# Optimization experiments

Measured on AMD Instinct MI355X. Metric: run time of the kernel, lower is better.

Reference implementation:

```python
import jax, jax.numpy as jnp
import numpy as np

# NOTE on reconstructed deps (not shown in source):
#  - utils.mmnorm(x): max-magnitude norm, x / (max|x| over last dim + eps)
#  - model.LearnableFourierResampler(din, dout, nf): x -> Linear(din,nf) -> [sin,cos] -> Linear(2nf,dout)
#  - utils.pscan(q, fn, identity): Hillis-Steele log-depth scan: for n in 1,2,4,...:
#        q = fn(x=q, y=shift_right(q, n, fill=identity))   (Scanner.forward(x, y) cats (y, x))

B, T, C, NF = 8, 2048, 1024, 64
EPS = 1e-6

def mmnorm(x):
    return x / (jnp.max(jnp.abs(x), axis=-1, keepdims=True) + EPS)

def setup_inputs() -> dict:
    key = jax.random.key(0)
    ks = jax.random.split(key, 8)
    def w(k, shape, fan_in):
        return jax.random.normal(k, shape, jnp.float32) * (1.0 / np.sqrt(fan_in))
    return {
        "x": jax.random.normal(ks[0], (B, T, C), jnp.float32),
        "attn_W": w(ks[1], (C, 2 * C), C),
        "attn_b": jnp.zeros((2 * C,), jnp.float32),
        "freq_W": w(ks[2], (2 * C, NF), 2 * C),
        "freq_b": jnp.zeros((NF,), jnp.float32),
        "out_W": w(ks[3], (2 * NF, C), 2 * NF),
        "out_b": jnp.zeros((C,), jnp.float32),
        "proj_W": w(ks[4], (C, C), C),
        "proj_b": jnp.zeros((C,), jnp.float32),
        "identity": jax.random.uniform(ks[5], (C,), jnp.float32),
    }

def _scanner(y, x, freq_W, freq_b, out_W, out_b):
    # Scanner.forward(x, y): z = cat((y, x)); Fourier resample; mmnorm
    z = jnp.concatenate([y, x], axis=-1)                      # [B,T,2C]
    f = z @ freq_W + freq_b                                   # [B,T,NF]
    z = jnp.concatenate([jnp.sin(f), jnp.cos(f)], -1) @ out_W + out_b  # [B,T,C]
    return mmnorm(z)

def reference(x, attn_W, attn_b, freq_W, freq_b, out_W, out_b, proj_W, proj_b, identity):
    b, t, c = x.shape
    qv = x @ attn_W + attn_b
    q, v = qv[..., :c], qv[..., c:]
    # Hillis-Steele parallel scan with nonlinear learned combine
    n = 1
    while n < t:
        prev = jnp.concatenate(
            [jnp.broadcast_to(identity, (b, n, c)), q[:, : t - n]], axis=1)
        q = _scanner(prev, q, freq_W, freq_b, out_W, out_b)
        n *= 2
    Y = q * v
    return Y @ proj_W + proj_b
```

## Files before the change

kernel.cpp:

```cpp
#include <hip/hip_runtime.h>
#include <hip/hip_bf16.h>
#include <math.h>


#define R_ROWS 16384
#define T_DIM  2048
#define C_DIM  1024

typedef unsigned short u16;
typedef __attribute__((ext_vector_type(8))) short short8;
typedef __attribute__((ext_vector_type(4))) float f32x4;

__device__ __forceinline__ u16 f2bf(float f) {
  union { float f; unsigned u; } v; v.f = f;
  unsigned r = v.u + 0x7fffu + ((v.u >> 16) & 1u);
  return (u16)(r >> 16);
}
__device__ __forceinline__ float bf2f(u16 h) {
  union { unsigned u; float f; } v; v.u = ((unsigned)h) << 16;
  return v.f;
}
__device__ __forceinline__ void gld16(const void* g, void* l) {
  __builtin_amdgcn_global_load_lds(
      (const __attribute__((address_space(1))) void*)g,
      (__attribute__((address_space(3))) void*)l, 16, 0, 0);
}

__global__ __launch_bounds__(256) void cvt_bf16(const float* __restrict__ in,
                                                u16* __restrict__ out, int n8) {
  const int i = blockIdx.x * 256 + threadIdx.x;
  if (i >= n8) return;
  const float4 a = ((const float4*)in)[2 * i];
  const float4 b = ((const float4*)in)[2 * i + 1];
  alignas(16) u16 t[8] = {f2bf(a.x), f2bf(a.y), f2bf(a.z), f2bf(a.w),
                          f2bf(b.x), f2bf(b.y), f2bf(b.z), f2bf(b.w)};
  ((uint4*)out)[i] = *(const uint4*)t;
}

__device__ __forceinline__ void cvtT_tile(const float* W, u16* Wt, int K, int N,
                                          int noff, int k0, int n0,
                                          float (*t)[33]) {
  const int tx = threadIdx.x & 31, ty = threadIdx.x >> 5;
#pragma unroll
  for (int i = 0; i < 32; i += 8)
    t[ty + i][tx] = W[(size_t)(k0 + ty + i) * N + noff + n0 + tx];
  __syncthreads();
#pragma unroll
  for (int i = 0; i < 32; i += 8)
    Wt[(size_t)(n0 + ty + i) * K + k0 + tx] = f2bf(t[tx][ty + i]);
}

__global__ __launch_bounds__(256) void prep_weights(
    const float* __restrict__ attn_W, const float* __restrict__ proj_W,
    const float* __restrict__ out_W, const float* __restrict__ freq_W,
    u16* __restrict__ aWt, u16* __restrict__ pWt, u16* __restrict__ w2t,
    u16* __restrict__ w1f, u16* __restrict__ Wqb, u16* __restrict__ Wob) {
  __shared__ float t[32][33];
  const int bid = blockIdx.x;
  if (bid < 1024) {
    cvtT_tile(attn_W, aWt, 1024, 2048, 1024, (bid & 31) * 32, (bid >> 5) * 32, t);
  } else if (bid < 2048) {
    const int b = bid - 1024;
    cvtT_tile(proj_W, pWt, 1024, 1024, 0, (b & 31) * 32, (b >> 5) * 32, t);
  } else if (bid < 2176) {
    const int b = bid - 2048;
    cvtT_tile(out_W, w2t, 128, 1024, 0, (b & 3) * 32, (b >> 2) * 32, t);
  } else if (bid < 2304) {
    const int b = bid - 2176;
    const int k0 = (b & 63) * 32, n0 = (b >> 6) * 32;
    const int tx = threadIdx.x & 31, ty = threadIdx.x >> 5;
#pragma unroll
    for (int i = 0; i < 32; i += 8)
      t[ty + i][tx] = freq_W[(size_t)(k0 + ty + i) * 64 + n0 + tx];
    __syncthreads();
#pragma unroll
    for (int i = 0; i < 32; i += 8) {
      const int k = k0 + tx;
      const int row = (n0 + ty + i) + ((k >= 1024) ? 64 : 0);
      w1f[(size_t)row * 1024 + (k & 1023)] = f2bf(t[tx][ty + i]);
    }
  } else if (bid < 3328) {
    const int c = bid - 2304, k0 = threadIdx.x * 4;
    const float4 a = *(const float4*)&attn_W[(size_t)c * 2048 + k0];
    alignas(8) u16 tt[4] = {f2bf(a.x), f2bf(a.y), f2bf(a.z), f2bf(a.w)};
    *(uint2*)&Wqb[(size_t)c * 1024 + k0] = *(const uint2*)tt;
  } else {
    const int c = bid - 3328, k0 = threadIdx.x * 4;
    const float4 a = *(const float4*)&out_W[(size_t)c * 1024 + k0];
    alignas(8) u16 tt[4] = {f2bf(a.x), f2bf(a.y), f2bf(a.z), f2bf(a.w)};
    *(uint2*)&Wob[(size_t)c * 1024 + k0] = *(const uint2*)tt;
  }
}

__device__ __forceinline__ void gm_body(const u16* w1f, const u16* B,
                                        u16* Mt, int ldO, int n0, u16* As) {
  const int tid = threadIdx.x, lane = tid & 63, w = tid >> 6;
  const int ln = lane & 15, qd = lane >> 4;
  const int wm = w & 1, wn = w >> 1;
  const int srow = w * 32 + (lane >> 3);
  const int scol = ((lane & 7) ^ ((lane >> 3) & 7)) * 8;
  f32x4 acc[4][2] = {};
  for (int kt = 0; kt < 1024; kt += 64) {
    __syncthreads();
#pragma unroll
    for (int j = 0; j < 4; j++)
      gld16(&w1f[(size_t)(srow + j * 8) * 1024 + kt + scol],
            &As[(w * 32 + j * 8) * 64]);
    __syncthreads();
#pragma unroll
    for (int ks = 0; ks < 2; ks++) {
      short8 af[4];
#pragma unroll
      for (int i = 0; i < 4; i++) {
        const int ar = wm * 64 + i * 16 + ln;
        af[i] = *(const short8*)&As[ar * 64 + ((ks * 4 + qd) ^ (ar & 7)) * 8];
      }
#pragma unroll
      for (int nt = 0; nt < 2; nt++) {
        const short8 b = *(const short8*)&B[(size_t)(n0 + wn * 32 + nt * 16 + ln) * 1024 +
                                            kt + ks * 32 + qd * 8];
#pragma unroll
        for (int i = 0; i < 4; i++)
          acc[i][nt] = __builtin_amdgcn_mfma_f32_16x16x32_bf16(af[i], b, acc[i][nt], 0, 0, 0);
      }
    }
  }
#pragma unroll
  for (int i = 0; i < 4; i++)
#pragma unroll
    for (int nt = 0; nt < 2; nt++)
#pragma unroll
      for (int r = 0; r < 4; r++)
        Mt[(size_t)(wm * 64 + i * 16 + qd * 4 + r) * ldO +
           n0 + wn * 32 + nt * 16 + ln] = f2bf(acc[i][nt][r]);
}

__device__ __forceinline__ void dotred_body(const float* ab, const u16* w1f,
                                            float* outv, float* red) {
  const int tid = threadIdx.x, j = tid >> 1, part = tid & 1;
  float s = 0.f;
  for (int k = part * 512; k < part * 512 + 512; k++)
    s += ab[k] * bf2f(w1f[(size_t)j * 1024 + k]);
  red[tid] = s;
  __syncthreads();
  if (part == 0) outv[j] = red[2 * j] + red[2 * j + 1];
}

__global__ __launch_bounds__(256) void prep_small(
    const float* __restrict__ ident, const float* __restrict__ freq_W,
    const float* __restrict__ attn_b, const float* __restrict__ out_b,
    const u16* __restrict__ w1f, const u16* __restrict__ Wqb,
    const u16* __restrict__ Wob, float* __restrict__ fid,
    float* __restrict__ bgv, float* __restrict__ c1,
    u16* __restrict__ Mt, u16* __restrict__ W21t) {
  __shared__ u16 sh[8192];
  float* red = (float*)sh;
  const int bid = blockIdx.x;
  if (bid == 0) {
    const int tid = threadIdx.x;
    const int j = tid >> 2, part = tid & 3;
    float s = 0.f;
    for (int k = part * 256; k < part * 256 + 256; k++)
      s += ident[k] * freq_W[(size_t)k * 64 + j];
    red[tid] = s;
    __syncthreads();
    if (part == 0) fid[j] = red[tid] + red[tid + 1] + red[tid + 2] + red[tid + 3];
  } else if (bid == 1) {
    dotred_body(attn_b, w1f, bgv, red);
  } else if (bid == 2) {
    dotred_body(out_b, w1f, c1, red);
  } else if (bid < 19) {
    gm_body(w1f, Wqb, Mt, 1024, (bid - 3) * 64, sh);
  } else {
    gm_body(w1f, Wob, W21t, 128, (bid - 19) * 64, sh);
  }
}

#define GEMM_KLOOP(Aptr, Bptr)                                                 \
  const int tid = threadIdx.x, lane = tid & 63, w = tid >> 6;                  \
  const int ln = lane & 15, qd = lane >> 4;                                    \
  const int wm = w & 1, wn = w >> 1;                                           \
  const int nbx = gridDim.x;                                                   \
  const int bid0 = blockIdx.y * nbx + blockIdx.x;                              \
  const int nwg = nbx * gridDim.y;                                             \
  const int bid = (bid0 & 7) * (nwg >> 3) + (bid0 >> 3);                       \
  const int n0 = (bid % nbx) * 128, m0 = (bid / nbx) * 128;                    \
  const int srow = w * 32 + (lane >> 3);                                       \
  const int sl = (lane & 7) ^ ((lane >> 3) & 7);                               \
  const int scol = sl * 8;                                                     \
  f32x4 acc[4][4] = {};                                                        \
  for (int kt = 0; kt < 1024; kt += 64) {                                      \
    __syncthreads();                                                           \
    _Pragma("unroll") for (int j = 0; j < 4; j++) {                            \
      gld16(&Aptr[(size_t)(m0 + srow + j * 8) * 1024 + kt + scol],             \
            &As[(w * 32 + j * 8) * 64]);                                       \
      gld16(&Bptr[(size_t)(n0 + srow + j * 8) * 1024 + kt + scol],             \
            &Bs[(w * 32 + j * 8) * 64]);                                       \
    }                                                                          \
    __syncthreads();                                                           \
    _Pragma("unroll") for (int ks = 0; ks < 2; ks++) {                         \
      short8 af[4], bf_[4];                                                    \
      _Pragma("unroll") for (int i = 0; i < 4; i++) {                          \
        const int ar = wm * 64 + i * 16 + ln;                                  \
        af[i] = *(const short8*)&As[ar * 64 + ((ks * 4 + qd) ^ (ar & 7)) * 8]; \
      }                                                                        \
      _Pragma("unroll") for (int j = 0; j < 4; j++) {                          \
        const int br = wn * 64 + j * 16 + ln;                                  \
        bf_[j] = *(const short8*)&Bs[br * 64 + ((ks * 4 + qd) ^ (br & 7)) * 8];\
      }                                                                        \
      _Pragma("unroll") for (int i = 0; i < 4; i++)                            \
      _Pragma("unroll") for (int j = 0; j < 4; j++)                            \
        acc[i][j] = __builtin_amdgcn_mfma_f32_16x16x32_bf16(af[i], bf_[j],     \
                                                            acc[i][j], 0, 0, 0);\
    }                                                                          \
  }                                                                            \
  __syncthreads();

__global__ __launch_bounds__(256) void gemm_vg_mfma(
    const u16* __restrict__ A, const u16* __restrict__ Bt,
    const float* __restrict__ bias, const float* __restrict__ bg,
    u16* __restrict__ Vb, float* __restrict__ G) {
  __shared__ u16 S[16384];
  u16* As = S;
  u16* Bs = S + 8192;
  GEMM_KLOOP(A, Bt)
  if (n0 < 1024) {
#pragma unroll
    for (int j = 0; j < 4; j++) {
      const int col = wn * 64 + j * 16 + ln;
      const float bv = bias[n0 + col];
#pragma unroll
      for (int i = 0; i < 4; i++)
#pragma unroll
        for (int r = 0; r < 4; r++)
          S[(wm * 64 + i * 16 + qd * 4 + r) * 128 + col] = f2bf(acc[i][j][r] + bv);
    }
    __syncthreads();
#pragma unroll
    for (int it = 0; it < 8; it++) {
      const int idx = it * 256 + tid;
      const int row = idx >> 4, seg = idx & 15;
      *(uint4*)&Vb[(size_t)(m0 + row) * 1024 + n0 + seg * 8] = ((const uint4*)S)[idx];
    }
  } else {
#pragma unroll
    for (int j = 0; j < 4; j++) {
      const int col = wn * 64 + j * 16 + ln;
      const float bv = bg[col];
#pragma unroll
      for (int i = 0; i < 4; i++)
#pragma unroll
        for (int r = 0; r < 4; r++)
          G[(size_t)(m0 + wm * 64 + i * 16 + qd * 4 + r) * 128 + col] =
              acc[i][j][r] + bv;
    }
  }
}

__global__ __launch_bounds__(256) void gemm_proj_mfma(
    const u16* __restrict__ A, const u16* __restrict__ Bt,
    const float* __restrict__ bias, float* __restrict__ OUT) {
  __shared__ u16 S[16384];
  u16* As = S;
  u16* Bs = S + 8192;
  GEMM_KLOOP(A, Bt)
  float* Csf = (float*)S;
#pragma unroll
  for (int p = 0; p < 2; p++) {
    if (wm == p) {
#pragma unroll
      for (int j = 0; j < 4; j++) {
        const int col = wn * 64 + j * 16 + ln;
        const float bv = bias[n0 + col];
#pragma unroll
        for (int i = 0; i < 4; i++)
#pragma unroll
          for (int r = 0; r < 4; r++)
            Csf[(i * 16 + qd * 4 + r) * 128 + col] = acc[i][j][r] + bv;
      }
    }
    __syncthreads();
#pragma unroll
    for (int it = 0; it < 8; it++) {
      const int idx = it * 256 + tid;
      const int row = idx >> 5, seg = idx & 31;
      *(uint4*)&OUT[(size_t)(m0 + p * 64 + row) * 1024 + n0 + seg * 4] =
          ((const uint4*)Csf)[idx];
    }
    __syncthreads();
  }
}

__global__ __launch_bounds__(1024, 4) void scan_fused(
    const float* __restrict__ Gsrc, float* __restrict__ Gdst,
    const u16* __restrict__ W21t, const u16* __restrict__ W2t,
    const float* __restrict__ b1, const float* __restrict__ b2,
    const float* __restrict__ fid, const float* __restrict__ c1,
    const u16* __restrict__ Vb, u16* __restrict__ Yout, int n, int flags) {
  __shared__ u16 S[64 * 128];
  __shared__ unsigned rmax[64];
  const int tid = threadIdx.x, lane = tid & 63, wv = tid >> 6;
  const int ln = lane & 15, qd = lane >> 4;
  const int bid = blockIdx.x;
  const int r0 = (((bid & 7) << 5) + (bid >> 3)) * 64;
  if (tid < 64) rmax[tid] = 0u;
  {
    const int r = tid >> 4, js = (tid & 15) << 2;
    const int gr = r0 + r, tl = gr & (T_DIM - 1);
    const float* g1p = (tl >= n) ? &Gsrc[(size_t)(gr - n) * 128 + js] : &fid[js];
    const float4 g1 = *(const float4*)g1p;
    const float4 g2 = *(const float4*)&Gsrc[(size_t)gr * 128 + 64 + js];
    const float4 bb = *(const float4*)&b1[js];
    float f[4] = {g1.x + g2.x + bb.x, g1.y + g2.y + bb.y,
                  g1.z + g2.z + bb.z, g1.w + g2.w + bb.w};
    alignas(8) u16 sn[4], cs[4];
#pragma unroll
    for (int c = 0; c < 4; c++) {
      float sv, cv;
      __sincosf(f[c], &sv, &cv);
      sn[c] = f2bf(sv);
      cs[c] = f2bf(cv);
    }
    const int u = js >> 3, half = (js >> 2) & 1, rx = r & 7;
    const int ps = (u ^ rx) & 7;
    const int pc = 8 | ps;
    *(uint2*)&S[r * 128 + ps * 8 + half * 4] = *(const uint2*)sn;
    *(uint2*)&S[r * 128 + pc * 8 + half * 4] = *(const uint2*)cs;
  }
  __syncthreads();
  const u16* w2b = W2t + (size_t)wv * 64 * 128;
  f32x4 acc[4][4] = {};
#pragma unroll
  for (int ks = 0; ks < 4; ks++) {
    short8 af[4];
#pragma unroll
    for (int i = 0; i < 4; i++) {
      const int ar = i * 16 + ln;
      const int u = ks * 4 + qd;
      af[i] = *(const short8*)&S[ar * 128 + ((u & 8) | ((u ^ ar) & 7)) * 8];
    }
#pragma unroll
    for (int nt = 0; nt < 4; nt++) {
      const short8 b = *(const short8*)&w2b[(size_t)(nt * 16 + ln) * 128 + ks * 32 + qd * 8];
#pragma unroll
      for (int i = 0; i < 4; i++)
        acc[i][nt] = __builtin_amdgcn_mfma_f32_16x16x32_bf16(b, af[i], acc[i][nt], 0, 0, 0);
    }
  }
  float mx[4] = {0.f, 0.f, 0.f, 0.f};
#pragma unroll
  for (int nt = 0; nt < 4; nt++) {
    const float4 bb = *(const float4*)&b2[wv * 64 + nt * 16 + qd * 4];
    const float br4[4] = {bb.x, bb.y, bb.z, bb.w};
#pragma unroll
    for (int i = 0; i < 4; i++)
#pragma unroll
      for (int r = 0; r < 4; r++) {
        const float v = acc[i][nt][r] + br4[r];
        acc[i][nt][r] = v;
        mx[i] = fmaxf(mx[i], fabsf(v));
      }
  }
#pragma unroll
  for (int i = 0; i < 4; i++) {
    float v = mx[i];
    v = fmaxf(v, __shfl_xor(v, 16, 64));
    v = fmaxf(v, __shfl_xor(v, 32, 64));
    if (lane < 16) atomicMax(&rmax[i * 16 + lane], __float_as_uint(v));
  }
  __syncthreads();
  if (flags & 1) {
    float inv[4];
#pragma unroll
    for (int i = 0; i < 4; i++)
      inv[i] = 1.0f / (__uint_as_float(rmax[i * 16 + ln]) + 1e-6f);
#pragma unroll
    for (int i = 0; i < 4; i++) {
      const int row = i * 16 + ln;
#pragma unroll
      for (int nt = 0; nt < 4; nt++) {
        const int col = wv * 64 + nt * 16 + qd * 4;
        const uint2 vv = *(const uint2*)&Vb[(size_t)(r0 + row) * 1024 + col];
        const u16* vp = (const u16*)&vv;
        uint2 pv;
        pv.x = (unsigned)f2bf(acc[i][nt][0] * inv[i] * bf2f(vp[0])) |
               ((unsigned)f2bf(acc[i][nt][1] * inv[i] * bf2f(vp[1])) << 16);
        pv.y = (unsigned)f2bf(acc[i][nt][2] * inv[i] * bf2f(vp[2])) |
               ((unsigned)f2bf(acc[i][nt][3] * inv[i] * bf2f(vp[3])) << 16);
        *(uint2*)&Yout[(size_t)(r0 + row) * 1024 + col] = pv;
      }
    }
  }
  if (flags & 2) {
    const int wm3 = wv & 3, wn3 = wv >> 2;
    f32x4 g[2] = {};
#pragma unroll
    for (int ks = 0; ks < 4; ks++) {
      const int ar = wm3 * 16 + ln;
      const int u = ks * 4 + qd;
      const short8 a = *(const short8*)&S[ar * 128 + ((u & 8) | ((u ^ ar) & 7)) * 8];
#pragma unroll
      for (int c = 0; c < 2; c++) {
        const short8 b = *(const short8*)&W21t[(size_t)(wn3 * 32 + c * 16 + ln) * 128 +
                                               ks * 32 + qd * 8];
        g[c] = __builtin_amdgcn_mfma_f32_16x16x32_bf16(a, b, g[c], 0, 0, 0);
      }
    }
#pragma unroll
    for (int c = 0; c < 2; c++) {
      const int col = wn3 * 32 + c * 16 + ln;
      const float cb = c1[col];
#pragma unroll
      for (int r = 0; r < 4; r++) {
        const int row = wm3 * 16 + qd * 4 + r;
        const float invr = 1.0f / (__uint_as_float(rmax[row]) + 1e-6f);
        Gdst[(size_t)(r0 + row) * 128 + col] = (g[c][r] + cb) * invr;
      }
    }
  }
}

extern "C" void kernel_launch(void* const* d_in, const int* in_sizes, int n_in,
                              void* d_out, int out_size, void* d_ws, size_t ws_size,
                              hipStream_t stream) {
  const float* x      = (const float*)d_in[0];
  const float* attn_W = (const float*)d_in[1];
  const float* attn_b = (const float*)d_in[2];
  const float* freq_W = (const float*)d_in[3];
  const float* freq_b = (const float*)d_in[4];
  const float* out_W  = (const float*)d_in[5];
  const float* out_b  = (const float*)d_in[6];
  const float* proj_W = (const float*)d_in[7];
  const float* proj_b = (const float*)d_in[8];
  const float* ident  = (const float*)d_in[9];
  float* out = (float*)d_out;

  const size_t RC = (size_t)R_ROWS * C_DIM;
  u16* Xb  = (u16*)d_ws;
  u16* Qb  = Xb + RC;
  u16* Wqb = Qb;
  u16* Wob = Qb + (size_t)1024 * 1024;
  u16* Vb  = Qb + RC;
  u16* aWt = Vb + RC;
  u16* Mt  = aWt + (size_t)1024 * 1024;
  u16* pWt = aWt + (size_t)2048 * 1024;
  u16* w2t = pWt + (size_t)1024 * 1024;
  u16* w1f = w2t + (size_t)1024 * 128;
  float* Ga  = (float*)(w1f + (size_t)128 * 1024);
  float* Gb  = Ga + (size_t)R_ROWS * 128;
  float* fid = Gb + (size_t)R_ROWS * 128;
  float* c1  = fid + 64;
  float* bgv = c1 + 128;
  u16* W21t  = (u16*)(bgv + 128);

  cvt_bf16<<<8192, 256, 0, stream>>>(x, Xb, (int)(RC / 8));
  prep_weights<<<3456, 256, 0, stream>>>(attn_W, proj_W, out_W, freq_W,
                                         aWt, pWt, w2t, w1f, Wqb, Wob);
  prep_small<<<21, 256, 0, stream>>>(ident, freq_W, attn_b, out_b, w1f, Wqb,
                                     Wob, fid, bgv, c1, Mt, W21t);

  gemm_vg_mfma<<<dim3(9, 128), 256, 0, stream>>>(Xb, aWt, attn_b + 1024, bgv,
                                                 Vb, Ga);

  float* gs = Ga;
  float* gd = Gb;
  for (int n = 1; n < 1024; n <<= 1) {
    scan_fused<<<256, 1024, 0, stream>>>(gs, gd, W21t, w2t, freq_b, out_b, fid,
                                         c1, Vb, Xb, n, 2);
    float* t = gs; gs = gd; gd = t;
  }
  scan_fused<<<256, 1024, 0, stream>>>(gs, gd, W21t, w2t, freq_b, out_b, fid,
                                       c1, Vb, Xb, 1024, 1);

  gemm_proj_mfma<<<dim3(8, 128), 256, 0, stream>>>(Xb, pWt, proj_b, out);
}
```

Before: 359.4 us.

## Fuse pairs of early scan steps into one kernel using halo rows in LDS

Adds a scan_pair kernel that runs two consecutive Hillis-Steele steps (n and 2n) for n=1,4,16 inside one launch. It keeps the intermediate 128-wide G state in shared memory with a 48-row halo, recomputing halo rows in the first step. This replaces six scan_fused launches with three, saving global round-trips of the G buffer and launch overhead. The cost is redundant compute on halo rows and a larger LDS footprint that may reduce occupancy.

```diff
diff --git a/kernel.cpp b/kernel.cpp
--- a/kernel.cpp
+++ b/kernel.cpp
@@ -6,6 +6,8 @@
 #define R_ROWS 16384
 #define T_DIM  2048
 #define C_DIM  1024
+#define SROWS  112
+#define GP     132
 
 typedef unsigned short u16;
 typedef __attribute__((ext_vector_type(8))) short short8;
@@ -291,6 +293,199 @@
   }
 }
 
+template <int NT>
+__device__ __forceinline__ void zpass(const u16* S, const u16* w2b,
+                                      const float* b2, unsigned* rmax,
+                                      int rb, int wv, int ln, int qd, int lane) {
+  f32x4 acc[NT][4] = {};
+#pragma unroll
+  for (int ks = 0; ks < 4; ks++) {
+    short8 b[4];
+#pragma unroll
+    for (int nt = 0; nt < 4; nt++)
+      b[nt] = *(const short8*)&w2b[(size_t)(nt * 16 + ln) * 128 + ks * 32 + qd * 8];
+    short8 af[NT];
+#pragma unroll
+    for (int i = 0; i < NT; i++) {
+      const int ar = rb + i * 16 + ln;
+      const int u = ks * 4 + qd;
+      af[i] = *(const short8*)&S[ar * 128 + ((u & 8) | ((u ^ ar) & 7)) * 8];
+    }
+#pragma unroll
+    for (int nt = 0; nt < 4; nt++)
+#pragma unroll
+      for (int i = 0; i < NT; i++)
+        acc[i][nt] = __builtin_amdgcn_mfma_f32_16x16x32_bf16(b[nt], af[i], acc[i][nt], 0, 0, 0);
+  }
+  float mx[NT];
+#pragma unroll
+  for (int i = 0; i < NT; i++) mx[i] = 0.f;
+#pragma unroll
+  for (int nt = 0; nt < 4; nt++) {
+    const float4 bb = *(const float4*)&b2[wv * 64 + nt * 16 + qd * 4];
+    const float br4[4] = {bb.x, bb.y, bb.z, bb.w};
+#pragma unroll
+    for (int i = 0; i < NT; i++)
+#pragma unroll
+      for (int r = 0; r < 4; r++)
+        mx[i] = fmaxf(mx[i], fabsf(acc[i][nt][r] + br4[r]));
+  }
+#pragma unroll
+  for (int i = 0; i < NT; i++) {
+    float v = mx[i];
+    v = fmaxf(v, __shfl_xor(v, 16, 64));
+    v = fmaxf(v, __shfl_xor(v, 32, 64));
+    if (lane < 16) atomicMax(&rmax[rb + i * 16 + lane], __float_as_uint(v));
+  }
+}
+
+__device__ __forceinline__ void gpass4(const u16* S, const u16* W21t,
+                                       const float* c1, const unsigned* rmax,
+                                       float* GS, int rb, int wv, int ln, int qd) {
+  const int wm = wv & 3, wn = wv >> 2;
+  f32x4 g[2] = {};
+#pragma unroll
+  for (int ks = 0; ks < 4; ks++) {
+    const int ar = rb + wm * 16 + ln;
+    const int u = ks * 4 + qd;
+    const short8 a = *(const short8*)&S[ar * 128 + ((u & 8) | ((u ^ ar) & 7)) * 8];
+#pragma unroll
+    for (int c = 0; c < 2; c++) {
+      const short8 b = *(const short8*)&W21t[(size_t)(wn * 32 + c * 16 + ln) * 128 +
+                                             ks * 32 + qd * 8];
+      g[c] = __builtin_amdgcn_mfma_f32_16x16x32_bf16(a, b, g[c], 0, 0, 0);
+    }
+  }
+#pragma unroll
+  for (int c = 0; c < 2; c++) {
+    const int col = wn * 32 + c * 16 + ln;
+    const float cb = c1[col];
+#pragma unroll
+    for (int r = 0; r < 4; r++) {
+      const int row = rb + wm * 16 + qd * 4 + r;
+      const float invr = 1.0f / (__uint_as_float(rmax[row]) + 1e-6f);
+      GS[row * GP + col] = (g[c][r] + cb) * invr;
+    }
+  }
+}
+
+__device__ __forceinline__ void gpass2(const u16* S, const u16* W21t,
+                                       const float* c1, const unsigned* rmax,
+                                       float* GS, int rb, int wv, int ln, int qd) {
+  const int wm = wv & 1, wn = wv >> 1;
+  f32x4 g = {};
+#pragma unroll
+  for (int ks = 0; ks < 4; ks++) {
+    const int ar = rb + wm * 16 + ln;
+    const int u = ks * 4 + qd;
+    const short8 a = *(const short8*)&S[ar * 128 + ((u & 8) | ((u ^ ar) & 7)) * 8];
+    const short8 b = *(const short8*)&W21t[(size_t)(wn * 16 + ln) * 128 +
+                                           ks * 32 + qd * 8];
+    g = __builtin_amdgcn_mfma_f32_16x16x32_bf16(a, b, g, 0, 0, 0);
+  }
+  const int col = wn * 16 + ln;
+  const float cb = c1[col];
+#pragma unroll
+  for (int r = 0; r < 4; r++) {
+    const int row = rb + wm * 16 + qd * 4 + r;
+    const float invr = 1.0f / (__uint_as_float(rmax[row]) + 1e-6f);
+    GS[row * GP + col] = (g[r] + cb) * invr;
+  }
+}
+
+__global__ __launch_bounds__(1024, 4) void scan_pair(
+    const float* __restrict__ Gsrc, float* __restrict__ Gdst,
+    const u16* __restrict__ W21t, const u16* __restrict__ W2t,
+    const float* __restrict__ b1, const float* __restrict__ b2,
+    const float* __restrict__ fid, const float* __restrict__ c1, int nA) {
+  __shared__ float GS[SROWS * GP];
+  __shared__ u16 S[SROWS * 128];
+  __shared__ unsigned rmax[SROWS];
+  const int tid = threadIdx.x, lane = tid & 63, wv = tid >> 6;
+  const int ln = lane & 15, qd = lane >> 4;
+  const int bid = blockIdx.x;
+  const int r0 = (((bid & 7) << 5) + (bid >> 3)) * 64;
+#pragma unroll
+  for (int it = 0; it < 4; it++) {
+    const int idx = it * 1024 + tid;
+    if (idx < SROWS * 32) {
+      const int row = idx >> 5, c4 = (idx & 31) << 2;
+      const int g = r0 - 48 + row;
+      float4 v = {0.f, 0.f, 0.f, 0.f};
+      if (g >= 0) v = *(const float4*)&Gsrc[(size_t)g * 128 + c4];
+      *(float4*)&GS[row * GP + c4] = v;
+    }
+  }
+  const u16* w2b = W2t + (size_t)wv * 64 * 128;
+  int n = nA;
+  for (int s = 0; s < 2; s++, n <<= 1) {
+    const int srBeg = s ? 48 : 16;
+    __syncthreads();
+    if (tid < SROWS) rmax[tid] = 0u;
+    {
+      const int sr = srBeg + (tid >> 3);
+      if (sr < SROWS) {
+        const int js = (tid & 7) << 3;
+        const int g = r0 - 48 + sr, tl = g & (T_DIM - 1);
+        float g1v[8];
+        if (tl >= n) {
+          const float* p = &GS[(sr - n) * GP + js];
+          const float4 a0 = *(const float4*)p;
+          const float4 a1 = *(const float4*)(p + 4);
+          g1v[0] = a0.x; g1v[1] = a0.y; g1v[2] = a0.z; g1v[3] = a0.w;
+          g1v[4] = a1.x; g1v[5] = a1.y; g1v[6] = a1.z; g1v[7] = a1.w;
+        } else {
+          const float4 a0 = *(const float4*)&fid[js];
+          const float4 a1 = *(const float4*)&fid[js + 4];
+          g1v[0] = a0.x; g1v[1] = a0.y; g1v[2] = a0.z; g1v[3] = a0.w;
+          g1v[4] = a1.x; g1v[5] = a1.y; g1v[6] = a1.z; g1v[7] = a1.w;
+        }
+        const float4 g2a = *(const float4*)&GS[sr * GP + 64 + js];
+        const float4 g2b = *(const float4*)&GS[sr * GP + 64 + js + 4];
+        const float4 ba = *(const float4*)&b1[js];
+        const float4 bb4 = *(const float4*)&b1[js + 4];
+        float f[8] = {g1v[0] + g2a.x + ba.x,  g1v[1] + g2a.y + ba.y,
+                      g1v[2] + g2a.z + ba.z,  g1v[3] + g2a.w + ba.w,
+                      g1v[4] + g2b.x + bb4.x, g1v[5] + g2b.y + bb4.y,
+                      g1v[6] + g2b.z + bb4.z, g1v[7] + g2b.w + bb4.w};
+        alignas(16) u16 sn[8], cs[8];
+#pragma unroll
+        for (int c = 0; c < 8; c++) {
+          float sv, cv;
+          __sincosf(f[c], &sv, &cv);
+          sn[c] = f2bf(sv);
+          cs[c] = f2bf(cv);
+        }
+        const int ps = ((js >> 3) ^ (sr & 7)) & 7;
+        *(uint4*)&S[sr * 128 + ps * 8] = *(const uint4*)sn;
+        *(uint4*)&S[sr * 128 + (8 | ps) * 8] = *(const uint4*)cs;
+      }
+    }
+    __syncthreads();
+    if (s == 0) {
+      zpass<4>(S, w2b, b2, rmax, 16, wv, ln, qd, lane);
+      zpass<2>(S, w2b, b2, rmax, 80, wv, ln, qd, lane);
+    } else {
+      zpass<4>(S, w2b, b2, rmax, 48, wv, ln, qd, lane);
+    }
+    __syncthreads();
+    if (s == 0) {
+      gpass4(S, W21t, c1, rmax, GS, 16, wv, ln, qd);
+      gpass2(S, W21t, c1, rmax, GS, 80, wv, ln, qd);
+    } else {
+      gpass4(S, W21t, c1, rmax, GS, 48, wv, ln, qd);
+    }
+  }
+  __syncthreads();
+#pragma unroll
+  for (int it = 0; it < 2; it++) {
+    const int idx = it * 1024 + tid;
+    const int row = idx >> 5, c4 = (idx & 31) << 2;
+    *(float4*)&Gdst[(size_t)(r0 + row) * 128 + c4] =
+        *(const float4*)&GS[(48 + row) * GP + c4];
+  }
+}
+
 __global__ __launch_bounds__(1024, 4) void scan_fused(
     const float* __restrict__ Gsrc, float* __restrict__ Gdst,
     const u16* __restrict__ W21t, const u16* __restrict__ W2t,
@@ -464,7 +659,12 @@
 
   float* gs = Ga;
   float* gd = Gb;
-  for (int n = 1; n < 1024; n <<= 1) {
+  for (int nA = 1; nA <= 16; nA <<= 2) {
+    scan_pair<<<256, 1024, 0, stream>>>(gs, gd, W21t, w2t, freq_b, out_b, fid,
+                                        c1, nA);
+    float* t = gs; gs = gd; gd = t;
+  }
+  for (int n = 64; n < 1024; n <<= 1) {
     scan_fused<<<256, 1024, 0, stream>>>(gs, gd, W21t, w2t, freq_b, out_b, fid,
                                          c1, Vb, Xb, n, 2);
     float* t = gs; gs = gd; gd = t;
```

New measurement: 484.4 us. 1.35x slower.
